# Performance work log

Hardware: AMD Instinct MI355X
Metric: run time of the kernel (lower is better)

The kernel has to match this reference:

```python
import jax, jax.numpy as jnp
import numpy as np

D_MODEL = 1024
NUM_HEADS = 16
D_K = D_MODEL // NUM_HEADS


def setup_inputs() -> dict:
    key = jax.random.key(0)
    ks = jax.random.split(key, 11)
    B, S = 2, 2048
    scale = 1.0 / np.sqrt(D_MODEL)
    inp = {
        "q": jax.random.normal(ks[0], (B, S, D_MODEL), jnp.float32),
        "k": jax.random.normal(ks[1], (B, S, D_MODEL), jnp.float32),
        "v": jax.random.normal(ks[2], (B, S, D_MODEL), jnp.float32),
        "wq": jax.random.normal(ks[3], (D_MODEL, D_MODEL), jnp.float32) * scale,
        "bq": jax.random.normal(ks[4], (D_MODEL,), jnp.float32) * 0.01,
        "wk": jax.random.normal(ks[5], (D_MODEL, D_MODEL), jnp.float32) * scale,
        "bk": jax.random.normal(ks[6], (D_MODEL,), jnp.float32) * 0.01,
        "wv": jax.random.normal(ks[7], (D_MODEL, D_MODEL), jnp.float32) * scale,
        "bv": jax.random.normal(ks[8], (D_MODEL,), jnp.float32) * 0.01,
        "wo": jax.random.normal(ks[9], (D_MODEL, D_MODEL), jnp.float32) * scale,
        "bo": jax.random.normal(ks[10], (D_MODEL,), jnp.float32) * 0.01,
    }
    return inp


def reference(q, k, v, wq, bq, wk, bk, wv, bv, wo, bo):
    B, S, _ = q.shape
    # Linear projections (torch Linear: x @ W.T + b). Weights stored [out, in].
    qh = (q @ wq.T + bq).reshape(B, S, NUM_HEADS, D_K).transpose(0, 2, 1, 3)  # [B,H,S,dk]
    kh = (k @ wk.T + bk).reshape(B, S, NUM_HEADS, D_K).transpose(0, 2, 1, 3)
    vh = (v @ wv.T + bv).reshape(B, S, NUM_HEADS, D_K).transpose(0, 2, 1, 3)
    scores = jnp.einsum("bhqd,bhkd->bhqk", qh, kh) / jnp.sqrt(jnp.asarray(D_K, qh.dtype))
    weights = jax.nn.softmax(scores, axis=-1)
    attn = jnp.einsum("bhqk,bhkd->bhqd", weights, vh)  # [B,H,S,dk]
    attn = attn.transpose(0, 2, 1, 3).reshape(B, S, D_MODEL)
    return attn @ wo.T + bo
```

## Files before the change

### kernel.cpp

```cpp
#include <hip/hip_runtime.h>

#define DM 1024
#define NH 16
#define DK 64
#define BB 2
#define SS 2048
#define MT (BB*SS)

typedef __attribute__((ext_vector_type(8))) short bf16x8;
typedef __attribute__((ext_vector_type(4))) float f32x4;

#define QSCALE 0.1803368801111191f
#define EXPC  (-14.426950408889634f)

__device__ __forceinline__ unsigned short f2bf(float f) {
    unsigned int u = __float_as_uint(f);
    u += 0x7FFF + ((u >> 16) & 1);
    return (unsigned short)(u >> 16);
}

__device__ __forceinline__ unsigned int cvt_pk_bf16(float lo, float hi) {
    unsigned int r;
    asm("v_cvt_pk_bf16_f32 %0, %1, %2" : "=v"(r) : "v"(lo), "v"(hi));
    return r;
}

__device__ __forceinline__ void gload16(const void* g, void* l) {
    __builtin_amdgcn_global_load_lds(
        (const __attribute__((address_space(1))) unsigned int*)g,
        (__attribute__((address_space(3))) unsigned int*)(unsigned int)(unsigned long long)l,
        16, 0, 0);
}

struct CvtArgs {
    const float* s[7];
    unsigned short* d[7];
    int n[7];
    float scl[7];
};

__global__ __launch_bounds__(256) void cvt_f32_bf16(CvtArgs a) {
    const int arr = blockIdx.y;
    const int i = (blockIdx.x * 256 + threadIdx.x) * 8;
    if (i >= a.n[arr]) return;
    const float sc = a.scl[arr];
    const float4* sp = (const float4*)(a.s[arr] + i);
    float4 x = sp[0], y = sp[1];
    union { unsigned short us[8]; uint4 u4; } r;
    r.us[0] = f2bf(x.x * sc); r.us[1] = f2bf(x.y * sc);
    r.us[2] = f2bf(x.z * sc); r.us[3] = f2bf(x.w * sc);
    r.us[4] = f2bf(y.x * sc); r.us[5] = f2bf(y.y * sc);
    r.us[6] = f2bf(y.z * sc); r.us[7] = f2bf(y.w * sc);
    *(uint4*)(a.d[arr] + i) = r.u4;
}

struct ProjArgs {
    const unsigned short* A[3];
    const unsigned short* B[3];
    const float* bias[3];
    unsigned short* out[3];
    float bscale[3];
};

__global__ __launch_bounds__(256) void proj3(ProjArgs pa) {
    __shared__ __align__(16) unsigned short As[128 * 32];
    __shared__ __align__(16) unsigned short Bs[128 * 32];

    const int z = blockIdx.y;
    const int bx = blockIdx.x;
    const int m0 = (z < 2 ? (bx >> 3) : (bx >> 5)) * 128;
    const int n0 = (z < 2 ? (bx & 7) : (bx & 31)) * 128;
    const unsigned short* A = pa.A[z];
    const unsigned short* B = pa.B[z];
    const float* bias = pa.bias[z];
    const float bsc = pa.bscale[z];
    unsigned short* out = pa.out[z];

    const int tid = (int)threadIdx.x;
    const int l = tid & 63;
    const int w = tid >> 6;
    const int wm = w >> 1, wn = w & 1;

    const int strow = l >> 2;
    const int sslot = (l & 3) ^ ((l >> 3) & 3);
    const int fr = l & 15, fj = l >> 4;
    const int swz = ((fj ^ ((fr >> 1) & 3)) << 4);

    const f32x4 zero = {0.f, 0.f, 0.f, 0.f};
    f32x4 acc[4][4];
    #pragma unroll
    for (int mf = 0; mf < 4; ++mf)
        #pragma unroll
        for (int nf = 0; nf < 4; ++nf) acc[mf][nf] = zero;

    for (int kt = 0; kt < DM; kt += 32) {
        #pragma unroll
        for (int t = 0; t < 2; ++t) {
            const int c = w * 2 + t;
            const int row = c * 16 + strow;
            gload16(A + (size_t)(m0 + row) * DM + kt + sslot * 8, (char*)As + c * 1024);
            gload16(B + (size_t)(n0 + row) * DM + kt + sslot * 8, (char*)Bs + c * 1024);
        }
        __syncthreads();
        bf16x8 af[4], bfr[4];
        #pragma unroll
        for (int mf = 0; mf < 4; ++mf)
            af[mf] = *(const bf16x8*)((const char*)As + (wm * 64 + mf * 16 + fr) * 64 + swz);
        #pragma unroll
        for (int nf = 0; nf < 4; ++nf)
            bfr[nf] = *(const bf16x8*)((const char*)Bs + (wn * 64 + nf * 16 + fr) * 64 + swz);
        #pragma unroll
        for (int mf = 0; mf < 4; ++mf)
            #pragma unroll
            for (int nf = 0; nf < 4; ++nf)
                acc[mf][nf] = __builtin_amdgcn_mfma_f32_16x16x32_bf16(af[mf], bfr[nf], acc[mf][nf], 0, 0, 0);
        __syncthreads();
    }

    #pragma unroll
    for (int nf = 0; nf < 4; ++nf) {
        const int n = n0 + wn * 64 + nf * 16 + fr;
        const float bn = (z == 2) ? 0.f : bias[n] * bsc;
        #pragma unroll
        for (int mf = 0; mf < 4; ++mf) {
            #pragma unroll
            for (int j = 0; j < 4; ++j) {
                const int m = m0 + wm * 64 + mf * 16 + fj * 4 + j;
                if (z < 2) {
                    const float val = acc[mf][nf][j] + bn;
                    out[((size_t)((m >> 11) * NH + (n >> 6)) * SS + (m & (SS - 1))) * DK + (n & 63)] = f2bf(val);
                } else {
                    const float val = acc[mf][nf][j] + bias[m];
                    out[(size_t)((n >> 11) * NH + (m >> 6)) * (SS * DK) + (size_t)(m & 63) * SS + (n & (SS - 1))] = f2bf(val);
                }
            }
        }
    }
}

__global__ __launch_bounds__(256) void gemm_out(
    const unsigned short* __restrict__ A,
    const unsigned short* __restrict__ B,
    const float* __restrict__ bias,
    float* __restrict__ out)
{
    __shared__ __align__(16) unsigned short As[128 * 32];
    __shared__ __align__(16) unsigned short Bs[64 * 32];

    const int tid = (int)threadIdx.x;
    const int l = tid & 63;
    const int w = tid >> 6;
    const int wm = w >> 1, wn = w & 1;
    const int m0 = blockIdx.x * 128, n0 = blockIdx.y * 64;

    const int strow = l >> 2;
    const int sslot = (l & 3) ^ ((l >> 3) & 3);
    const int fr = l & 15, fj = l >> 4;
    const int swz = ((fj ^ ((fr >> 1) & 3)) << 4);

    const f32x4 zero = {0.f, 0.f, 0.f, 0.f};
    f32x4 acc[4][2];
    #pragma unroll
    for (int mf = 0; mf < 4; ++mf)
        #pragma unroll
        for (int nf = 0; nf < 2; ++nf) acc[mf][nf] = zero;

    for (int kt = 0; kt < DM; kt += 32) {
        #pragma unroll
        for (int t = 0; t < 2; ++t) {
            const int c = w * 2 + t;
            gload16(A + (size_t)(m0 + c * 16 + strow) * DM + kt + sslot * 8, (char*)As + c * 1024);
        }
        gload16(B + (size_t)(n0 + w * 16 + strow) * DM + kt + sslot * 8, (char*)Bs + w * 1024);
        __syncthreads();
        bf16x8 af[4], bfr[2];
        #pragma unroll
        for (int mf = 0; mf < 4; ++mf)
            af[mf] = *(const bf16x8*)((const char*)As + (wm * 64 + mf * 16 + fr) * 64 + swz);
        #pragma unroll
        for (int nf = 0; nf < 2; ++nf)
            bfr[nf] = *(const bf16x8*)((const char*)Bs + (wn * 32 + nf * 16 + fr) * 64 + swz);
        #pragma unroll
        for (int mf = 0; mf < 4; ++mf)
            #pragma unroll
            for (int nf = 0; nf < 2; ++nf)
                acc[mf][nf] = __builtin_amdgcn_mfma_f32_16x16x32_bf16(af[mf], bfr[nf], acc[mf][nf], 0, 0, 0);
        __syncthreads();
    }

    #pragma unroll
    for (int nf = 0; nf < 2; ++nf) {
        const int n = n0 + wn * 32 + nf * 16 + fr;
        const float bn = bias[n];
        #pragma unroll
        for (int mf = 0; mf < 4; ++mf)
            #pragma unroll
            for (int j = 0; j < 4; ++j) {
                const int m = m0 + wm * 64 + mf * 16 + fj * 4 + j;
                out[(size_t)m * DM + n] = acc[mf][nf][j] + bn;
            }
    }
}

__global__ __launch_bounds__(256) void attn_bf16(
    const unsigned short* __restrict__ qh,
    const unsigned short* __restrict__ kh,
    const unsigned short* __restrict__ vt,
    unsigned short* __restrict__ ao)
{
    __shared__ __align__(16) unsigned short Qs[128 * 64];
    __shared__ __align__(16) unsigned short Ks[2][64 * 64];
    __shared__ __align__(16) unsigned short Vs[2][64 * 64];
    __shared__ __align__(16) unsigned short Ps[128 * 64];

    const int tid = (int)threadIdx.x;
    const int l = tid & 63;
    const int w = tid >> 6;
    const int bh = blockIdx.y;
    const int q0 = blockIdx.x * 128;
    const size_t pb = (size_t)bh * (SS * DK);

    const int fr = l & 15, fj = l >> 4;
    const int s8 = fr & 7;
    const int strow = l >> 3;
    const int sslot = (l & 7) ^ strow;

    #pragma unroll
    for (int t = 0; t < 4; ++t) {
        const int c = w * 4 + t;
        gload16(qh + pb + (size_t)(q0 + c * 8 + strow) * DK + sslot * 8, (char*)Qs + c * 1024);
    }
    #pragma unroll
    for (int t = 0; t < 2; ++t) {
        const int c = w * 2 + t;
        gload16(kh + pb + (size_t)(c * 8 + strow) * DK + sslot * 8, (char*)Ks[0] + c * 1024);
        gload16(vt + pb + (size_t)(c * 8 + strow) * SS + sslot * 8, (char*)Vs[0] + c * 1024);
    }
    __syncthreads();

    const f32x4 zero = {0.f, 0.f, 0.f, 0.f};
    f32x4 o[2][4];
    f32x4 lacc[2];
    #pragma unroll
    for (int mf = 0; mf < 2; ++mf)
        #pragma unroll
        for (int nf = 0; nf < 4; ++nf) o[mf][nf] = zero;
    lacc[0] = zero; lacc[1] = zero;

    const int NT = SS / 64;
    for (int t = 0; t < NT; ++t) {
        const int c = t & 1;
        if (t + 1 < NT) {
            #pragma unroll
            for (int tt = 0; tt < 2; ++tt) {
                const int ch = w * 2 + tt;
                gload16(kh + pb + (size_t)((t + 1) * 64 + ch * 8 + strow) * DK + sslot * 8,
                        (char*)Ks[c ^ 1] + ch * 1024);
            }
        }
        f32x4 sc[4][2];
        #pragma unroll
        for (int kf = 0; kf < 4; ++kf)
            #pragma unroll
            for (int qf = 0; qf < 2; ++qf) sc[kf][qf] = zero;
        __builtin_amdgcn_s_setprio(1);
        #pragma unroll
        for (int ks = 0; ks < 2; ++ks) {
            bf16x8 kfr[4], qfr[2];
            #pragma unroll
            for (int kf = 0; kf < 4; ++kf)
                kfr[kf] = *(const bf16x8*)((const char*)Ks[c] + (kf * 16 + fr) * 128 + (((ks * 4 + fj) ^ s8) << 4));
            #pragma unroll
            for (int qf = 0; qf < 2; ++qf)
                qfr[qf] = *(const bf16x8*)((const char*)Qs + (w * 32 + qf * 16 + fr) * 128 + (((ks * 4 + fj) ^ s8) << 4));
            #pragma unroll
            for (int kf = 0; kf < 4; ++kf)
                #pragma unroll
                for (int qf = 0; qf < 2; ++qf)
                    sc[kf][qf] = __builtin_amdgcn_mfma_f32_16x16x32_bf16(kfr[kf], qfr[qf], sc[kf][qf], 0, 0, 0);
        }
        __builtin_amdgcn_s_setprio(0);

        __builtin_amdgcn_sched_barrier(0);
        __builtin_amdgcn_s_barrier();
        __builtin_amdgcn_sched_barrier(0);

        if (t + 1 < NT) {
            #pragma unroll
            for (int tt = 0; tt < 2; ++tt) {
                const int ch = w * 2 + tt;
                gload16(vt + pb + (size_t)(ch * 8 + strow) * SS + (t + 1) * 64 + sslot * 8,
                        (char*)Vs[c ^ 1] + ch * 1024);
            }
        }

        #pragma unroll
        for (int qf = 0; qf < 2; ++qf) {
            const int qq = w * 32 + qf * 16 + fr;
            #pragma unroll
            for (int kf = 0; kf < 4; ++kf) {
                const float e0 = __builtin_amdgcn_exp2f(sc[kf][qf][0] + EXPC);
                const float e1 = __builtin_amdgcn_exp2f(sc[kf][qf][1] + EXPC);
                const float e2 = __builtin_amdgcn_exp2f(sc[kf][qf][2] + EXPC);
                const float e3 = __builtin_amdgcn_exp2f(sc[kf][qf][3] + EXPC);
                lacc[qf][0] += e0; lacc[qf][1] += e1;
                lacc[qf][2] += e2; lacc[qf][3] += e3;
                uint2 pw;
                pw.x = cvt_pk_bf16(e0, e1);
                pw.y = cvt_pk_bf16(e2, e3);
                *(uint2*)((char*)Ps + qq * 128 + (((2 * kf + (fj >> 1)) ^ s8) << 4) + ((fj & 1) << 3)) = pw;
            }
        }

        __builtin_amdgcn_sched_barrier(0);
        if (t + 1 < NT) asm volatile("s_waitcnt vmcnt(2) lgkmcnt(0)" ::: "memory");
        else            asm volatile("s_waitcnt vmcnt(0) lgkmcnt(0)" ::: "memory");
        __builtin_amdgcn_s_barrier();
        __builtin_amdgcn_sched_barrier(0);

        __builtin_amdgcn_s_setprio(1);
        #pragma unroll
        for (int kp = 0; kp < 2; ++kp) {
            bf16x8 pf[2], vf[4];
            #pragma unroll
            for (int mf = 0; mf < 2; ++mf)
                pf[mf] = *(const bf16x8*)((const char*)Ps + (w * 32 + mf * 16 + fr) * 128 + (((kp * 4 + fj) ^ s8) << 4));
            #pragma unroll
            for (int nf = 0; nf < 4; ++nf)
                vf[nf] = *(const bf16x8*)((const char*)Vs[c] + (nf * 16 + fr) * 128 + (((kp * 4 + fj) ^ s8) << 4));
            #pragma unroll
            for (int mf = 0; mf < 2; ++mf)
                #pragma unroll
                for (int nf = 0; nf < 4; ++nf)
                    o[mf][nf] = __builtin_amdgcn_mfma_f32_16x16x32_bf16(pf[mf], vf[nf], o[mf][nf], 0, 0, 0);
        }
        __builtin_amdgcn_s_setprio(0);
    }

    float inv[2];
    #pragma unroll
    for (int qf = 0; qf < 2; ++qf) {
        float s = (lacc[qf][0] + lacc[qf][1]) + (lacc[qf][2] + lacc[qf][3]);
        s += __shfl_xor(s, 16);
        s += __shfl_xor(s, 32);
        inv[qf] = 1.0f / s;
    }
    const int b = bh >> 4, h = bh & 15;
    #pragma unroll
    for (int mf = 0; mf < 2; ++mf) {
        float iv[4];
        #pragma unroll
        for (int j = 0; j < 4; ++j) iv[j] = __shfl(inv[mf], fj * 4 + j);
        #pragma unroll
        for (int nf = 0; nf < 4; ++nf) {
            const int d = nf * 16 + fr;
            #pragma unroll
            for (int j = 0; j < 4; ++j) {
                const int qg = q0 + w * 32 + mf * 16 + fj * 4 + j;
                ao[(size_t)(b * SS + qg) * DM + h * DK + d] = f2bf(o[mf][nf][j] * iv[j]);
            }
        }
    }
}

extern "C" void kernel_launch(void* const* d_in, const int* in_sizes, int n_in,
                              void* d_out, int out_size, void* d_ws, size_t ws_size,
                              hipStream_t stream) {
    const float* q  = (const float*)d_in[0];
    const float* k  = (const float*)d_in[1];
    const float* v  = (const float*)d_in[2];
    const float* wq = (const float*)d_in[3];
    const float* bq = (const float*)d_in[4];
    const float* wk = (const float*)d_in[5];
    const float* bk = (const float*)d_in[6];
    const float* wv = (const float*)d_in[7];
    const float* bv = (const float*)d_in[8];
    const float* wo = (const float*)d_in[9];
    const float* bo = (const float*)d_in[10];

    const size_t NQ = (size_t)MT * DM;
    const size_t NW = (size_t)DM * DM;
    unsigned short* wsb = (unsigned short*)d_ws;
    unsigned short* qb  = wsb;
    unsigned short* kb  = qb  + NQ;
    unsigned short* vb  = kb  + NQ;
    unsigned short* wqb = vb  + NQ;
    unsigned short* wkb = wqb + NW;
    unsigned short* wvb = wkb + NW;
    unsigned short* wob = wvb + NW;
    unsigned short* qhb = wob + NW;
    unsigned short* khb = qhb + NQ;
    unsigned short* vtb = khb + NQ;
    unsigned short* aob = vtb + NQ;

    CvtArgs ca;
    ca.s[0] = q;  ca.d[0] = qb;  ca.n[0] = (int)NQ; ca.scl[0] = 1.f;
    ca.s[1] = k;  ca.d[1] = kb;  ca.n[1] = (int)NQ; ca.scl[1] = 1.f;
    ca.s[2] = v;  ca.d[2] = vb;  ca.n[2] = (int)NQ; ca.scl[2] = 1.f;
    ca.s[3] = wq; ca.d[3] = wqb; ca.n[3] = (int)NW; ca.scl[3] = QSCALE;
    ca.s[4] = wk; ca.d[4] = wkb; ca.n[4] = (int)NW; ca.scl[4] = 1.f;
    ca.s[5] = wv; ca.d[5] = wvb; ca.n[5] = (int)NW; ca.scl[5] = 1.f;
    ca.s[6] = wo; ca.d[6] = wob; ca.n[6] = (int)NW; ca.scl[6] = 1.f;
    cvt_f32_bf16<<<dim3(2048, 7), dim3(256), 0, stream>>>(ca);

    ProjArgs pa;
    pa.A[0] = qb;  pa.B[0] = wqb; pa.bias[0] = bq; pa.out[0] = qhb; pa.bscale[0] = QSCALE;
    pa.A[1] = kb;  pa.B[1] = wkb; pa.bias[1] = bk; pa.out[1] = khb; pa.bscale[1] = 1.f;
    pa.A[2] = wvb; pa.B[2] = vb;  pa.bias[2] = bv; pa.out[2] = vtb; pa.bscale[2] = 1.f;
    proj3<<<dim3(256, 3), dim3(256), 0, stream>>>(pa);

    attn_bf16<<<dim3(16, 32), dim3(256), 0, stream>>>(qhb, khb, vtb, aob);

    gemm_out<<<dim3(32, 16), dim3(256), 0, stream>>>(aob, wob, bo, (float*)d_out);
}
```

Before: 136.9 us.

## Double-buffer GEMM LDS tiles and enlarge attention query tile with Q in registers

Both projection GEMMs get two LDS buffers. The next K-slice is prefetched while MFMAs run on the current one, which halves the barriers per iteration. The attention kernel now handles 256 queries per block and keeps Q fragments in registers instead of LDS, so each K/V tile is reused over twice as many queries. The cost is half as many attention blocks and higher register pressure per wave. Launch-bounds occupancy hints are added to all three kernels.

```diff
diff --git a/kernel.cpp b/kernel.cpp
--- a/kernel.cpp
+++ b/kernel.cpp
@@ -62,9 +62,9 @@
     float bscale[3];
 };
 
-__global__ __launch_bounds__(256) void proj3(ProjArgs pa) {
-    __shared__ __align__(16) unsigned short As[128 * 32];
-    __shared__ __align__(16) unsigned short Bs[128 * 32];
+__global__ __launch_bounds__(256, 3) void proj3(ProjArgs pa) {
+    __shared__ __align__(16) unsigned short As[2][128 * 32];
+    __shared__ __align__(16) unsigned short Bs[2][128 * 32];
 
     const int z = blockIdx.y;
     const int bx = blockIdx.x;
@@ -93,22 +93,33 @@
         #pragma unroll
         for (int nf = 0; nf < 4; ++nf) acc[mf][nf] = zero;
 
+    #pragma unroll
+    for (int t = 0; t < 2; ++t) {
+        const int c = w * 2 + t;
+        const int row = c * 16 + strow;
+        gload16(A + (size_t)(m0 + row) * DM + sslot * 8, (char*)As[0] + c * 1024);
+        gload16(B + (size_t)(n0 + row) * DM + sslot * 8, (char*)Bs[0] + c * 1024);
+    }
+    __syncthreads();
+
     for (int kt = 0; kt < DM; kt += 32) {
-        #pragma unroll
-        for (int t = 0; t < 2; ++t) {
-            const int c = w * 2 + t;
-            const int row = c * 16 + strow;
-            gload16(A + (size_t)(m0 + row) * DM + kt + sslot * 8, (char*)As + c * 1024);
-            gload16(B + (size_t)(n0 + row) * DM + kt + sslot * 8, (char*)Bs + c * 1024);
-        }
-        __syncthreads();
+        const int cb = (kt >> 5) & 1;
+        if (kt + 32 < DM) {
+            #pragma unroll
+            for (int t = 0; t < 2; ++t) {
+                const int c = w * 2 + t;
+                const int row = c * 16 + strow;
+                gload16(A + (size_t)(m0 + row) * DM + (kt + 32) + sslot * 8, (char*)As[cb ^ 1] + c * 1024);
+                gload16(B + (size_t)(n0 + row) * DM + (kt + 32) + sslot * 8, (char*)Bs[cb ^ 1] + c * 1024);
+            }
+        }
         bf16x8 af[4], bfr[4];
         #pragma unroll
         for (int mf = 0; mf < 4; ++mf)
-            af[mf] = *(const bf16x8*)((const char*)As + (wm * 64 + mf * 16 + fr) * 64 + swz);
+            af[mf] = *(const bf16x8*)((const char*)As[cb] + (wm * 64 + mf * 16 + fr) * 64 + swz);
         #pragma unroll
         for (int nf = 0; nf < 4; ++nf)
-            bfr[nf] = *(const bf16x8*)((const char*)Bs + (wn * 64 + nf * 16 + fr) * 64 + swz);
+            bfr[nf] = *(const bf16x8*)((const char*)Bs[cb] + (wn * 64 + nf * 16 + fr) * 64 + swz);
         #pragma unroll
         for (int mf = 0; mf < 4; ++mf)
             #pragma unroll
@@ -138,14 +149,14 @@
     }
 }
 
-__global__ __launch_bounds__(256) void gemm_out(
+__global__ __launch_bounds__(256, 2) void gemm_out(
     const unsigned short* __restrict__ A,
     const unsigned short* __restrict__ B,
     const float* __restrict__ bias,
     float* __restrict__ out)
 {
-    __shared__ __align__(16) unsigned short As[128 * 32];
-    __shared__ __align__(16) unsigned short Bs[64 * 32];
+    __shared__ __align__(16) unsigned short As[2][128 * 32];
+    __shared__ __align__(16) unsigned short Bs[2][64 * 32];
 
     const int tid = (int)threadIdx.x;
     const int l = tid & 63;
@@ -165,21 +176,31 @@
         #pragma unroll
         for (int nf = 0; nf < 2; ++nf) acc[mf][nf] = zero;
 
+    #pragma unroll
+    for (int t = 0; t < 2; ++t) {
+        const int c = w * 2 + t;
+        gload16(A + (size_t)(m0 + c * 16 + strow) * DM + sslot * 8, (char*)As[0] + c * 1024);
+    }
+    gload16(B + (size_t)(n0 + w * 16 + strow) * DM + sslot * 8, (char*)Bs[0] + w * 1024);
+    __syncthreads();
+
     for (int kt = 0; kt < DM; kt += 32) {
-        #pragma unroll
-        for (int t = 0; t < 2; ++t) {
-            const int c = w * 2 + t;
-            gload16(A + (size_t)(m0 + c * 16 + strow) * DM + kt + sslot * 8, (char*)As + c * 1024);
-        }
-        gload16(B + (size_t)(n0 + w * 16 + strow) * DM + kt + sslot * 8, (char*)Bs + w * 1024);
-        __syncthreads();
+        const int cb = (kt >> 5) & 1;
+        if (kt + 32 < DM) {
+            #pragma unroll
+            for (int t = 0; t < 2; ++t) {
+                const int c = w * 2 + t;
+                gload16(A + (size_t)(m0 + c * 16 + strow) * DM + (kt + 32) + sslot * 8, (char*)As[cb ^ 1] + c * 1024);
+            }
+            gload16(B + (size_t)(n0 + w * 16 + strow) * DM + (kt + 32) + sslot * 8, (char*)Bs[cb ^ 1] + w * 1024);
+        }
         bf16x8 af[4], bfr[2];
         #pragma unroll
         for (int mf = 0; mf < 4; ++mf)
-            af[mf] = *(const bf16x8*)((const char*)As + (wm * 64 + mf * 16 + fr) * 64 + swz);
+            af[mf] = *(const bf16x8*)((const char*)As[cb] + (wm * 64 + mf * 16 + fr) * 64 + swz);
         #pragma unroll
         for (int nf = 0; nf < 2; ++nf)
-            bfr[nf] = *(const bf16x8*)((const char*)Bs + (wn * 32 + nf * 16 + fr) * 64 + swz);
+            bfr[nf] = *(const bf16x8*)((const char*)Bs[cb] + (wn * 32 + nf * 16 + fr) * 64 + swz);
         #pragma unroll
         for (int mf = 0; mf < 4; ++mf)
             #pragma unroll
@@ -202,22 +223,21 @@
     }
 }
 
-__global__ __launch_bounds__(256) void attn_bf16(
+__global__ __launch_bounds__(256, 1) void attn_bf16(
     const unsigned short* __restrict__ qh,
     const unsigned short* __restrict__ kh,
     const unsigned short* __restrict__ vt,
     unsigned short* __restrict__ ao)
 {
-    __shared__ __align__(16) unsigned short Qs[128 * 64];
     __shared__ __align__(16) unsigned short Ks[2][64 * 64];
     __shared__ __align__(16) unsigned short Vs[2][64 * 64];
-    __shared__ __align__(16) unsigned short Ps[128 * 64];
+    __shared__ __align__(16) unsigned short Ps[256 * 64];
 
     const int tid = (int)threadIdx.x;
     const int l = tid & 63;
     const int w = tid >> 6;
     const int bh = blockIdx.y;
-    const int q0 = blockIdx.x * 128;
+    const int q0 = blockIdx.x * 256;
     const size_t pb = (size_t)bh * (SS * DK);
 
     const int fr = l & 15, fj = l >> 4;
@@ -225,11 +245,13 @@
     const int strow = l >> 3;
     const int sslot = (l & 7) ^ strow;
 
-    #pragma unroll
-    for (int t = 0; t < 4; ++t) {
-        const int c = w * 4 + t;
-        gload16(qh + pb + (size_t)(q0 + c * 8 + strow) * DK + sslot * 8, (char*)Qs + c * 1024);
-    }
+    bf16x8 qreg[4][2];
+    #pragma unroll
+    for (int qf = 0; qf < 4; ++qf)
+        #pragma unroll
+        for (int ks = 0; ks < 2; ++ks)
+            qreg[qf][ks] = *(const bf16x8*)(qh + pb + (size_t)(q0 + w * 64 + qf * 16 + fr) * DK + ks * 32 + fj * 8);
+
     #pragma unroll
     for (int t = 0; t < 2; ++t) {
         const int c = w * 2 + t;
@@ -239,13 +261,14 @@
     __syncthreads();
 
     const f32x4 zero = {0.f, 0.f, 0.f, 0.f};
-    f32x4 o[2][4];
-    f32x4 lacc[2];
-    #pragma unroll
-    for (int mf = 0; mf < 2; ++mf)
+    f32x4 o[4][4];
+    f32x4 lacc[4];
+    #pragma unroll
+    for (int mf = 0; mf < 4; ++mf) {
         #pragma unroll
         for (int nf = 0; nf < 4; ++nf) o[mf][nf] = zero;
-    lacc[0] = zero; lacc[1] = zero;
+        lacc[mf] = zero;
+    }
 
     const int NT = SS / 64;
     for (int t = 0; t < NT; ++t) {
@@ -258,26 +281,23 @@
                         (char*)Ks[c ^ 1] + ch * 1024);
             }
         }
-        f32x4 sc[4][2];
+        f32x4 sc[4][4];
         #pragma unroll
         for (int kf = 0; kf < 4; ++kf)
             #pragma unroll
-            for (int qf = 0; qf < 2; ++qf) sc[kf][qf] = zero;
+            for (int qf = 0; qf < 4; ++qf) sc[kf][qf] = zero;
         __builtin_amdgcn_s_setprio(1);
         #pragma unroll
         for (int ks = 0; ks < 2; ++ks) {
-            bf16x8 kfr[4], qfr[2];
+            bf16x8 kfr[4];
             #pragma unroll
             for (int kf = 0; kf < 4; ++kf)
                 kfr[kf] = *(const bf16x8*)((const char*)Ks[c] + (kf * 16 + fr) * 128 + (((ks * 4 + fj) ^ s8) << 4));
             #pragma unroll
-            for (int qf = 0; qf < 2; ++qf)
-                qfr[qf] = *(const bf16x8*)((const char*)Qs + (w * 32 + qf * 16 + fr) * 128 + (((ks * 4 + fj) ^ s8) << 4));
-            #pragma unroll
             for (int kf = 0; kf < 4; ++kf)
                 #pragma unroll
-                for (int qf = 0; qf < 2; ++qf)
-                    sc[kf][qf] = __builtin_amdgcn_mfma_f32_16x16x32_bf16(kfr[kf], qfr[qf], sc[kf][qf], 0, 0, 0);
+                for (int qf = 0; qf < 4; ++qf)
+                    sc[kf][qf] = __builtin_amdgcn_mfma_f32_16x16x32_bf16(kfr[kf], qreg[qf][ks], sc[kf][qf], 0, 0, 0);
         }
         __builtin_amdgcn_s_setprio(0);
 
@@ -295,8 +315,8 @@
         }
 
         #pragma unroll
-        for (int qf = 0; qf < 2; ++qf) {
-            const int qq = w * 32 + qf * 16 + fr;
+        for (int qf = 0; qf < 4; ++qf) {
+            const int qq = w * 64 + qf * 16 + fr;
             #pragma unroll
             for (int kf = 0; kf < 4; ++kf) {
                 const float e0 = __builtin_amdgcn_exp2f(sc[kf][qf][0] + EXPC);
@@ -321,15 +341,15 @@
         __builtin_amdgcn_s_setprio(1);
         #pragma unroll
         for (int kp = 0; kp < 2; ++kp) {
-            bf16x8 pf[2], vf[4];
-            #pragma unroll
-            for (int mf = 0; mf < 2; ++mf)
-                pf[mf] = *(const bf16x8*)((const char*)Ps + (w * 32 + mf * 16 + fr) * 128 + (((kp * 4 + fj) ^ s8) << 4));
+            bf16x8 pf[4], vf[4];
+            #pragma unroll
+            for (int mf = 0; mf < 4; ++mf)
+                pf[mf] = *(const bf16x8*)((const char*)Ps + (w * 64 + mf * 16 + fr) * 128 + (((kp * 4 + fj) ^ s8) << 4));
             #pragma unroll
             for (int nf = 0; nf < 4; ++nf)
                 vf[nf] = *(const bf16x8*)((const char*)Vs[c] + (nf * 16 + fr) * 128 + (((kp * 4 + fj) ^ s8) << 4));
             #pragma unroll
-            for (int mf = 0; mf < 2; ++mf)
+            for (int mf = 0; mf < 4; ++mf)
                 #pragma unroll
                 for (int nf = 0; nf < 4; ++nf)
                     o[mf][nf] = __builtin_amdgcn_mfma_f32_16x16x32_bf16(pf[mf], vf[nf], o[mf][nf], 0, 0, 0);
@@ -337,9 +357,9 @@
         __builtin_amdgcn_s_setprio(0);
     }
 
-    float inv[2];
-    #pragma unroll
-    for (int qf = 0; qf < 2; ++qf) {
+    float inv[4];
+    #pragma unroll
+    for (int qf = 0; qf < 4; ++qf) {
         float s = (lacc[qf][0] + lacc[qf][1]) + (lacc[qf][2] + lacc[qf][3]);
         s += __shfl_xor(s, 16);
         s += __shfl_xor(s, 32);
@@ -347,7 +367,7 @@
     }
     const int b = bh >> 4, h = bh & 15;
     #pragma unroll
-    for (int mf = 0; mf < 2; ++mf) {
+    for (int mf = 0; mf < 4; ++mf) {
         float iv[4];
         #pragma unroll
         for (int j = 0; j < 4; ++j) iv[j] = __shfl(inv[mf], fj * 4 + j);
@@ -356,7 +376,7 @@
             const int d = nf * 16 + fr;
             #pragma unroll
             for (int j = 0; j < 4; ++j) {
-                const int qg = q0 + w * 32 + mf * 16 + fj * 4 + j;
+                const int qg = q0 + w * 64 + mf * 16 + fj * 4 + j;
                 ao[(size_t)(b * SS + qg) * DM + h * DK + d] = f2bf(o[mf][nf][j] * iv[j]);
             }
         }
@@ -409,7 +429,7 @@
     pa.A[2] = wvb; pa.B[2] = vb;  pa.bias[2] = bv; pa.out[2] = vtb; pa.bscale[2] = 1.f;
     proj3<<<dim3(256, 3), dim3(256), 0, stream>>>(pa);
 
-    attn_bf16<<<dim3(16, 32), dim3(256), 0, stream>>>(qhb, khb, vtb, aob);
+    attn_bf16<<<dim3(8, 32), dim3(256), 0, stream>>>(qhb, khb, vtb, aob);
 
     gemm_out<<<dim3(32, 16), dim3(256), 0, stream>>>(aob, wob, bo, (float*)d_out);
 }
```

After: 142.5 us. +4.1%, slower.
